# Optimization experiments

Hardware: AMD Instinct MI355X
Metric: run time of the kernel (lower is better)

## Reference

```python
import jax, jax.numpy as jnp
import numpy as np

B, HW, ENC, E, D, A, V, L = 64, 14, 2048, 512, 512, 512, 32000, 32
LN_EPS = 1e-5


def setup_inputs() -> dict:
    key = jax.random.key(0)
    ks = jax.random.split(key, 16)
    s = 0.02
    n = lambda k, sh: jax.random.normal(k, sh, jnp.float32)
    encoder_out = n(ks[0], (B, HW, HW, ENC))
    encoded_captions = jax.random.randint(ks[1], (B, L), 0, V)
    caption_lengths = jax.random.randint(ks[2], (B, 1), 2, L + 1)
    caption_lengths = caption_lengths.at[0, 0].set(L)  # ensure max length present
    return dict(
        encoder_out=encoder_out,
        encoded_captions=encoded_captions,
        caption_lengths=caption_lengths,
        emb=n(ks[3], (V, E)) * s,
        W_enc_att=n(ks[4], (A, ENC)) * s, b_enc_att=jnp.zeros((A,)),
        W_dec_att=n(ks[5], (A, D)) * s, b_dec_att=jnp.zeros((A,)),
        W_full_att=n(ks[6], (1, A)) * s, b_full_att=jnp.zeros((1,)),
        W_ih=n(ks[7], (4 * D, E + ENC)) * s, b_ih=jnp.zeros((4 * D,)),
        W_hh=n(ks[8], (4 * D, D)) * s, b_hh=jnp.zeros((4 * D,)),
        g_h=jnp.ones((D,)), be_h=jnp.zeros((D,)),
        g_c=jnp.ones((D,)), be_c=jnp.zeros((D,)),
        W_init_h=n(ks[9], (D, ENC)) * s, b_init_h=jnp.zeros((D,)),
        W_init_c=n(ks[10], (D, ENC)) * s, b_init_c=jnp.zeros((D,)),
        W_beta=n(ks[11], (ENC, D)) * s, b_beta=jnp.zeros((ENC,)),
        W_fc=n(ks[12], (V, D)) * s, b_fc=jnp.zeros((V,)),
    )


def _layer_norm(x, g, b):
    m = x.mean(-1, keepdims=True)
    v = ((x - m) ** 2).mean(-1, keepdims=True)
    return (x - m) / jnp.sqrt(v + LN_EPS) * g + b


def reference(encoder_out, encoded_captions, caption_lengths, emb,
              W_enc_att, b_enc_att, W_dec_att, b_dec_att, W_full_att, b_full_att,
              W_ih, b_ih, W_hh, b_hh, g_h, be_h, g_c, be_c,
              W_init_h, b_init_h, W_init_c, b_init_c, W_beta, b_beta, W_fc, b_fc):
    bsz = encoder_out.shape[0]
    enc_out = encoder_out.reshape(bsz, -1, encoder_out.shape[-1])  # [B,P,ENC]
    lengths = caption_lengths[:, 0]
    order = jnp.argsort(-lengths)  # stable descending sort (matches torch sort)
    lengths = lengths[order]
    enc_out = enc_out[order]
    caps = encoded_captions[order]
    embeds = emb[caps]  # [B,L,E]
    decode_lengths = lengths - 1
    T = caps.shape[1] - 1  # static max(decode_lengths)

    mean_enc = enc_out.mean(axis=1)
    h = _layer_norm(mean_enc @ W_init_h.T + b_init_h, g_h, be_h)
    c = _layer_norm(mean_enc @ W_init_c.T + b_init_c, g_c, be_c)

    att1 = enc_out @ W_enc_att.T + b_enc_att  # [B,P,A] precomputed once
    prev_seq = jnp.swapaxes(embeds[:, :T], 0, 1)  # [T,B,E] teacher-forced inputs
    masks = jnp.arange(T)[:, None] < decode_lengths[None, :]  # [T,B] active rows

    def step(carry, xs):
        h, c = carry
        prev, mask = xs
        # attention
        att2 = h @ W_dec_att.T + b_dec_att  # [B,A]
        e = jax.nn.relu(att1 + att2[:, None, :]) @ W_full_att[0] + b_full_att[0]  # [B,P]
        alpha = jax.nn.softmax(e, axis=1)
        awe = jnp.einsum('bpe,bp->be', enc_out, alpha)  # [B,ENC]
        gate = jax.nn.sigmoid(h @ W_beta.T + b_beta)
        awe = gate * awe
        # LSTM cell
        x = jnp.concatenate([prev, awe], axis=1)  # [B,E+ENC]
        gates = x @ W_ih.T + b_ih + h @ W_hh.T + b_hh
        i, f, g, o = jnp.split(gates, 4, axis=1)
        c_new = jax.nn.sigmoid(f) * c + jax.nn.sigmoid(i) * jnp.tanh(g)
        h_new = jax.nn.sigmoid(o) * jnp.tanh(c_new)
        h_new = _layer_norm(h_new, g_h, be_h)
        c_new = _layer_norm(c_new, g_c, be_c)
        preds = h_new @ W_fc.T + b_fc  # [B,V]; dropout is identity in eval
        m = mask[:, None]
        h = jnp.where(m, h_new, h)  # freeze finished rows (== torch batch shrink)
        c = jnp.where(m, c_new, c)
        return (h, c), (jnp.where(m, preds, 0.0), jnp.where(m, alpha, 0.0))

    (_, _), (preds_t, alphas_t) = jax.lax.scan(step, (h, c), (prev_seq, masks))
    predictions = jnp.swapaxes(preds_t, 0, 1)  # [B,T,V]
    alphas = jnp.swapaxes(alphas_t, 0, 1)      # [B,T,P]
    return predictions, caps, decode_lengths, alphas, order
```

## Files before the change

kernel.cpp:

```cpp
#include <hip/hip_runtime.h>
#include <cfloat>
#include <math.h>

#define B_ 64
#define P_ 196
#define ENC_ 2048
#define D_ 512
#define V_ 32000
#define L_ 32
#define T_ 31

#define OUT_PREDS 0L
#define OUT_CAPS  63488000L
#define OUT_DECL  63490048L
#define OUT_ALPH  63490112L
#define OUT_ORDER 63878976L

typedef __bf16 bf16;
typedef __bf16 bf16x8 __attribute__((ext_vector_type(8)));
typedef __bf16 bf16x4 __attribute__((ext_vector_type(4)));
typedef __bf16 bf16x2 __attribute__((ext_vector_type(2)));
typedef float  f32x4  __attribute__((ext_vector_type(4)));

static __device__ __forceinline__ float sigmoidf_(float x) { return 1.f / (1.f + __expf(-x)); }

__global__ void k_order(const int* __restrict__ cap_len, const int* __restrict__ caps,
                        int* __restrict__ order_i, int* __restrict__ declen_i,
                        int* __restrict__ caps_i, float* __restrict__ out,
                        int* __restrict__ rmap, int* __restrict__ orow, int* __restrict__ mact)
{
    __shared__ int len_s[B_], dl_s[B_];
    int tid = threadIdx.x;
    len_s[tid] = cap_len[tid];
    __syncthreads();
    int li = len_s[tid];
    int pos = 0;
    for (int j = 0; j < B_; ++j) {
        int lj = len_s[j];
        pos += (lj > li) || (lj == li && j < tid);
    }
    order_i[pos]  = tid;
    declen_i[pos] = li - 1;
    dl_s[pos]     = li - 1;
    out[OUT_ORDER + pos] = (float)tid;
    out[OUT_DECL  + pos] = (float)(li - 1);
    for (int l = 0; l < L_; ++l) {
        int tok = caps[tid * L_ + l];
        caps_i[pos * L_ + l] = tok;
        out[OUT_CAPS + pos * L_ + l] = (float)tok;
    }
    __syncthreads();
    int p = tid;
    int off = 0;
    for (int j = 0; j < p; ++j) off += dl_s[j];
    int dl = dl_s[p];
    for (int tt = 0; tt < dl; ++tt) {
        rmap[off + tt] = tt * B_ + p;
        orow[off + tt] = p * T_ + tt;
    }
    if (p == B_ - 1) {
        int M = off + dl;
        mact[0] = M;
        int Mr = (M + 63) & ~63;
        for (int i = M; i < Mr; ++i) { rmap[i] = 0; orow[i] = -1; }
    }
}

struct CvtSegs { const float* s[8]; bf16* d[8]; long cum[9]; };
__global__ __launch_bounds__(256) void k_cvt_all(CvtSegs cs)
{
    long i8 = ((long)blockIdx.x * 256 + threadIdx.x) * 8;
    if (i8 >= cs.cum[8]) return;
    int k = 0;
    while (i8 >= cs.cum[k + 1]) ++k;
    long loc = i8 - cs.cum[k];
    const float* src = cs.s[k] + loc;
    float4 a = *(const float4*)(src);
    float4 b = *(const float4*)(src + 4);
    bf16x8 v;
    v[0]=(bf16)a.x; v[1]=(bf16)a.y; v[2]=(bf16)a.z; v[3]=(bf16)a.w;
    v[4]=(bf16)b.x; v[5]=(bf16)b.y; v[6]=(bf16)b.z; v[7]=(bf16)b.w;
    *(bf16x8*)(cs.d[k] + loc) = v;
}

__global__ __launch_bounds__(256) void k_cvt_enc(const float* __restrict__ enc,
                                                 const int* __restrict__ order_i,
                                                 bf16* __restrict__ enc_s)
{
    long i = ((long)blockIdx.x * 256 + threadIdx.x) * 8;
    int b = (int)(i / ((long)P_ * ENC_));
    long rem = i - (long)b * P_ * ENC_;
    const float* src = enc + (long)order_i[b] * P_ * ENC_ + rem;
    float4 a = *(const float4*)(src);
    float4 c = *(const float4*)(src + 4);
    bf16x8 v;
    v[0]=(bf16)a.x; v[1]=(bf16)a.y; v[2]=(bf16)a.z; v[3]=(bf16)a.w;
    v[4]=(bf16)c.x; v[5]=(bf16)c.y; v[6]=(bf16)c.z; v[7]=(bf16)c.w;
    *(bf16x8*)(enc_s + i) = v;
}

__global__ __launch_bounds__(256) void k_meanb(const bf16* __restrict__ enc_s, bf16* __restrict__ mean_b)
{
    int b = blockIdx.x, col = blockIdx.y * 256 + threadIdx.x;
    float s = 0.f;
    const bf16* eb = enc_s + (long)b * P_ * ENC_ + col;
    for (int p = 0; p < P_; ++p) s += (float)eb[(long)p * ENC_];
    mean_b[(long)b * ENC_ + col] = (bf16)(s * (1.f / (float)P_));
}

template<int MI, int FUSE, int EPI, int SWZ>
__global__ void __launch_bounds__(256)
k_mgemm(const bf16* __restrict__ A, long lda,
        const bf16* __restrict__ B1, const bf16* __restrict__ B2,
        const float* __restrict__ bias,
        float* __restrict__ Cf, bf16* __restrict__ Cb,
        int N, int K, int kspl, int Nsp, int Ksp, int Mtot)
{
    const int tid = threadIdx.x;
    const int lane = tid & 63, w = tid >> 6;
    int mt, nt, z;
    if (SWZ == 0) { mt = blockIdx.x; nt = blockIdx.y; z = blockIdx.z; }
    else          { int o = blockIdx.x; int wg = (o & 7) * 196 + (o >> 3);
                    mt = wg >> 3; nt = (wg >> 1) & 3; z = wg & 1; }
    const int krange = K / kspl;
    const int k0 = z * krange, k1 = k0 + krange;
    const int r16 = lane & 15, kq = lane >> 4;
    const int koff = kq * 8;

    const bf16* Ap = A + (long)(mt * (MI * 16) + r16) * lda + koff;
    const int ncol0 = nt * 128 + w * 32;

    const bf16* Bp[2];
    const bf16* B2p[2];
#pragma unroll
    for (int ni = 0; ni < 2; ++ni) {
        int n = ncol0 + ni * 16 + r16;
        if (FUSE == 1)
            Bp[ni] = (n < Nsp) ? B1 + (long)n * K + koff
                               : B2 + (long)(n - Nsp) * K + koff;
        else if (FUSE == 2) {
            Bp[ni]  = B1 + (long)n * Ksp + koff;
            B2p[ni] = B2 + (long)n * (K - Ksp) + koff - Ksp;
        } else
            Bp[ni] = B1 + (long)n * K + koff;
    }

    auto loadA = [&](int kk, bf16x8* dst) {
#pragma unroll
        for (int mi = 0; mi < MI; ++mi)
            dst[mi] = *(const bf16x8*)(Ap + (long)mi * 16 * lda + kk);
    };
    auto loadB = [&](int kk, bf16x8* dst) {
#pragma unroll
        for (int ni = 0; ni < 2; ++ni) {
            if (FUSE == 2 && kk >= Ksp) dst[ni] = *(const bf16x8*)(B2p[ni] + kk);
            else                        dst[ni] = *(const bf16x8*)(Bp[ni] + kk);
        }
    };

    f32x4 acc[MI][2] = {};
    bf16x8 af[MI], bfr[2];
    loadA(k0, af); loadB(k0, bfr);
    for (int kk = k0 + 32; kk < k1; kk += 32) {
        bf16x8 af2[MI], bf2[2];
        loadA(kk, af2); loadB(kk, bf2);
#pragma unroll
        for (int mi = 0; mi < MI; ++mi)
#pragma unroll
            for (int ni = 0; ni < 2; ++ni)
                acc[mi][ni] = __builtin_amdgcn_mfma_f32_16x16x32_bf16(bfr[ni], af[mi], acc[mi][ni], 0, 0, 0);
#pragma unroll
        for (int mi = 0; mi < MI; ++mi) af[mi] = af2[mi];
#pragma unroll
        for (int ni = 0; ni < 2; ++ni) bfr[ni] = bf2[ni];
    }
#pragma unroll
    for (int mi = 0; mi < MI; ++mi)
#pragma unroll
        for (int ni = 0; ni < 2; ++ni)
            acc[mi][ni] = __builtin_amdgcn_mfma_f32_16x16x32_bf16(bfr[ni], af[mi], acc[mi][ni], 0, 0, 0);

#pragma unroll
    for (int mi = 0; mi < MI; ++mi) {
        const int row = mt * (MI * 16) + mi * 16 + r16;
#pragma unroll
        for (int ni = 0; ni < 2; ++ni) {
            const int col = ncol0 + ni * 16 + kq * 4;
            f32x4 v = acc[mi][ni];
            if (EPI == 0) {
                *(f32x4*)(Cf + (long)z * Mtot * N + (long)row * N + col) = v;
            } else {
                f32x4 bv = *(const f32x4*)(bias + col);
                bf16x4 o;
                o[0]=(bf16)(v[0]+bv[0]); o[1]=(bf16)(v[1]+bv[1]);
                o[2]=(bf16)(v[2]+bv[2]); o[3]=(bf16)(v[3]+bv[3]);
                *(bf16x4*)(Cb + (long)row * N + col) = o;
            }
        }
    }
}

__global__ __launch_bounds__(256)
void k_red(const float* __restrict__ p, const float* __restrict__ bias, bf16* __restrict__ ob)
{
    const long TOT = (long)12544 * 512;
    long i = ((long)blockIdx.x * 256 + threadIdx.x) * 8;
    f32x4 a0 = *(const f32x4*)(p + i);
    f32x4 a1 = *(const f32x4*)(p + i + 4);
    f32x4 b0 = *(const f32x4*)(p + TOT + i);
    f32x4 b1 = *(const f32x4*)(p + TOT + i + 4);
    int col = (int)(i & 511);
    f32x4 c0 = *(const f32x4*)(bias + col);
    f32x4 c1 = *(const f32x4*)(bias + col + 4);
    bf16x8 v;
    v[0]=(bf16)(a0[0]+b0[0]+c0[0]); v[1]=(bf16)(a0[1]+b0[1]+c0[1]);
    v[2]=(bf16)(a0[2]+b0[2]+c0[2]); v[3]=(bf16)(a0[3]+b0[3]+c0[3]);
    v[4]=(bf16)(a1[0]+b1[0]+c1[0]); v[5]=(bf16)(a1[1]+b1[1]+c1[1]);
    v[6]=(bf16)(a1[2]+b1[2]+c1[2]); v[7]=(bf16)(a1[3]+b1[3]+c1[3]);
    *(bf16x8*)(ob + i) = v;
}

__global__ __launch_bounds__(512)
void k_initln(const float* __restrict__ pi,
              const float* __restrict__ b_h, const float* __restrict__ b_c,
              const float* __restrict__ g_h, const float* __restrict__ be_h,
              const float* __restrict__ g_c, const float* __restrict__ be_c,
              bf16* __restrict__ xh, float* __restrict__ cbuf)
{
    int b = blockIdx.x, d = threadIdx.x;
    float yh = pi[(long)b * 1024 + d]       + b_h[d];
    float yc = pi[(long)b * 1024 + 512 + d] + b_c[d];
    __shared__ float r1[512], r2[512], r3[512], r4[512];
    r1[d] = yh; r2[d] = yh * yh; r3[d] = yc; r4[d] = yc * yc;
    __syncthreads();
    for (int s = 256; s > 0; s >>= 1) {
        if (d < s) { r1[d]+=r1[d+s]; r2[d]+=r2[d+s]; r3[d]+=r3[d+s]; r4[d]+=r4[d+s]; }
        __syncthreads();
    }
    float mh = r1[0] * (1.f/512.f), vh = r2[0] * (1.f/512.f) - mh*mh;
    float mc = r3[0] * (1.f/512.f), vc = r4[0] * (1.f/512.f) - mc*mc;
    float hln = (yh - mh) * rsqrtf(vh + 1e-5f) * g_h[d] + be_h[d];
    float cln = (yc - mc) * rsqrtf(vc + 1e-5f) * g_c[d] + be_c[d];
    xh[(long)b * 3072 + 2560 + d] = (bf16)hln;
    cbuf[(long)b * 512 + d] = cln;
}

__global__ __launch_bounds__(512)
void k_attn(const float* __restrict__ att2gate, const float* __restrict__ b_dec,
            const float* __restrict__ b_beta, const float* __restrict__ Wfull,
            const bf16* __restrict__ att1_b, const bf16* __restrict__ enc_s,
            const int* __restrict__ caps_i, const int* __restrict__ declen_i,
            const float* __restrict__ emb,
            bf16* __restrict__ xh, float* __restrict__ out, int t)
{
    const int b = blockIdx.x >> 1, seg = blockIdx.x & 1, tid = threadIdx.x;
    if (t >= declen_i[b]) {
        if (seg == 1 && tid < P_) out[OUT_ALPH + ((long)b * T_ + t) * P_ + tid] = 0.f;
        return;
    }
    __shared__ float att2s[512], wf[512], red[512], alp[P_];
    {
        float s = b_dec[tid];
#pragma unroll
        for (int zz = 0; zz < 4; ++zz) s += att2gate[((long)zz * 64 + b) * 2560 + tid];
        att2s[tid] = s;
        wf[tid] = Wfull[tid];
    }
    __syncthreads();
    float ev = -FLT_MAX;
    if (tid < P_) {
        const bf16* ar = att1_b + ((long)b * P_ + tid) * 512;
        float acc = 0.f;
        for (int a0 = 0; a0 < 512; a0 += 8) {
            bf16x8 v = *(const bf16x8*)(ar + a0);
#pragma unroll
            for (int j = 0; j < 8; ++j)
                acc += fmaxf((float)v[j] + att2s[a0 + j], 0.f) * wf[a0 + j];
        }
        ev = acc;
    }
    red[tid] = ev;
    __syncthreads();
    for (int s = 256; s > 0; s >>= 1) { if (tid < s) red[tid] = fmaxf(red[tid], red[tid + s]); __syncthreads(); }
    float mx = red[0];
    __syncthreads();
    float ex = (tid < P_) ? __expf(ev - mx) : 0.f;
    red[tid] = ex;
    __syncthreads();
    for (int s = 256; s > 0; s >>= 1) { if (tid < s) red[tid] += red[tid + s]; __syncthreads(); }
    float inv = 1.f / red[0];
    if (tid < P_) alp[tid] = ex * inv;
    __syncthreads();
    if (seg == 1 && tid < P_)
        out[OUT_ALPH + ((long)b * T_ + t) * P_ + tid] = alp[tid];
    const int c0 = seg * 1024 + tid * 2;
    const bf16* eb = enc_s + (long)b * P_ * ENC_ + c0;
    float a0 = 0.f, a1 = 0.f;
#pragma unroll 4
    for (int p = 0; p < P_; ++p) {
        bf16x2 v = *(const bf16x2*)(eb + (long)p * ENC_);
        float al = alp[p];
        a0 += al * (float)v[0]; a1 += al * (float)v[1];
    }
    float g0 = b_beta[c0], g1 = b_beta[c0 + 1];
#pragma unroll
    for (int zz = 0; zz < 4; ++zz) {
        const float* gs = att2gate + ((long)zz * 64 + b) * 2560 + 512 + c0;
        g0 += gs[0]; g1 += gs[1];
    }
    bf16x2 o;
    o[0] = (bf16)(a0 * sigmoidf_(g0));
    o[1] = (bf16)(a1 * sigmoidf_(g1));
    *(bf16x2*)(xh + (long)b * 3072 + 512 + c0) = o;
    if (seg == 0) {
        int tok = caps_i[b * L_ + t];
        xh[(long)b * 3072 + tid] = (bf16)emb[(long)tok * 512 + tid];
    }
}

__global__ __launch_bounds__(512)
void k_lstm(const float* __restrict__ gp, const float* __restrict__ b_ih, const float* __restrict__ b_hh,
            const float* __restrict__ g_h, const float* __restrict__ be_h,
            const float* __restrict__ g_c, const float* __restrict__ be_c,
            bf16* __restrict__ xh, float* __restrict__ cbuf, bf16* __restrict__ hseq,
            const int* __restrict__ declen_i, int t)
{
    int b = blockIdx.x, d = threadIdx.x;
    if (t >= declen_i[b]) return;
    float iv = b_ih[d]        + b_hh[d];
    float fv = b_ih[512 + d]  + b_hh[512 + d];
    float gv = b_ih[1024 + d] + b_hh[1024 + d];
    float ov = b_ih[1536 + d] + b_hh[1536 + d];
#pragma unroll
    for (int s = 0; s < 8; ++s) {
        const float* gs = gp + ((long)s * B_ + b) * 2048;
        iv += gs[d]; fv += gs[512 + d]; gv += gs[1024 + d]; ov += gs[1536 + d];
    }
    float cn = sigmoidf_(fv) * cbuf[(long)b * 512 + d] + sigmoidf_(iv) * tanhf(gv);
    float hn = sigmoidf_(ov) * tanhf(cn);
    __shared__ float r1[512], r2[512], r3[512], r4[512];
    r1[d] = hn; r2[d] = hn * hn; r3[d] = cn; r4[d] = cn * cn;
    __syncthreads();
    for (int s = 256; s > 0; s >>= 1) {
        if (d < s) { r1[d]+=r1[d+s]; r2[d]+=r2[d+s]; r3[d]+=r3[d+s]; r4[d]+=r4[d+s]; }
        __syncthreads();
    }
    float mh = r1[0] * (1.f/512.f), vh = r2[0] * (1.f/512.f) - mh*mh;
    float mc = r3[0] * (1.f/512.f), vc = r4[0] * (1.f/512.f) - mc*mc;
    float hln = (hn - mh) * rsqrtf(vh + 1e-5f) * g_h[d] + be_h[d];
    float cln = (cn - mc) * rsqrtf(vc + 1e-5f) * g_c[d] + be_c[d];
    bf16 hv = (bf16)hln;
    xh[(long)b * 3072 + 2560 + d] = hv;
    hseq[((long)t * B_ + b) * 512 + d] = hv;
    cbuf[(long)b * 512 + d] = cln;
}

__global__ __launch_bounds__(256) void k_zero(const int* __restrict__ declen_i, float* __restrict__ out)
{
    int x = blockIdx.x;
    int b = x / T_, t = x - b * T_;
    if (t < declen_i[b]) return;
    float4 z = {0.f, 0.f, 0.f, 0.f};
    long base = OUT_PREDS + ((long)b * T_ + t) * V_;
    for (int i = threadIdx.x * 4; i < V_; i += 1024)
        *(float4*)(out + base + i) = z;
}

__global__ __launch_bounds__(256)
void k_preds(const bf16* __restrict__ hseq, const bf16* __restrict__ Wfc,
             const float* __restrict__ bias,
             const int* __restrict__ rmap, const int* __restrict__ orow,
             const int* __restrict__ mact, float* __restrict__ out)
{
    int o = blockIdx.x; int xcd = o & 7;
    int base = xcd < 6 ? xcd * 969 : 5814 + (xcd - 6) * 968;
    int wg = base + (o >> 3);
    int nt = wg / 31, mt = wg - 31 * nt;
    if (mt * 64 >= mact[0]) return;
    __shared__ int rs[64], os[64];
    __shared__ __align__(16) float ct[64][132];
    const int tid = threadIdx.x, lane = tid & 63, w = tid >> 6;
    const int r16 = lane & 15, kq = lane >> 4, koff = kq * 8;
    if (tid < 64) { rs[tid] = rmap[mt * 64 + tid]; os[tid] = orow[mt * 64 + tid]; }
    __syncthreads();
    const int ncol0 = nt * 128 + w * 32;
    const bf16* Ap[4];
#pragma unroll
    for (int mi = 0; mi < 4; ++mi)
        Ap[mi] = hseq + (long)rs[mi * 16 + r16] * 512 + koff;
    const bf16* Bp[2];
#pragma unroll
    for (int ni = 0; ni < 2; ++ni)
        Bp[ni] = Wfc + (long)(ncol0 + ni * 16 + r16) * 512 + koff;

    f32x4 acc[4][2] = {};
    bf16x8 af[4], bfr[2];
#pragma unroll
    for (int mi = 0; mi < 4; ++mi) af[mi] = *(const bf16x8*)(Ap[mi]);
#pragma unroll
    for (int ni = 0; ni < 2; ++ni) bfr[ni] = *(const bf16x8*)(Bp[ni]);
    for (int kk = 32; kk < 512; kk += 32) {
        bf16x8 af2[4], bf2[2];
#pragma unroll
        for (int mi = 0; mi < 4; ++mi) af2[mi] = *(const bf16x8*)(Ap[mi] + kk);
#pragma unroll
        for (int ni = 0; ni < 2; ++ni) bf2[ni] = *(const bf16x8*)(Bp[ni] + kk);
#pragma unroll
        for (int mi = 0; mi < 4; ++mi)
#pragma unroll
            for (int ni = 0; ni < 2; ++ni)
                acc[mi][ni] = __builtin_amdgcn_mfma_f32_16x16x32_bf16(bfr[ni], af[mi], acc[mi][ni], 0, 0, 0);
#pragma unroll
        for (int mi = 0; mi < 4; ++mi) af[mi] = af2[mi];
#pragma unroll
        for (int ni = 0; ni < 2; ++ni) bfr[ni] = bf2[ni];
    }
#pragma unroll
    for (int mi = 0; mi < 4; ++mi)
#pragma unroll
        for (int ni = 0; ni < 2; ++ni)
            acc[mi][ni] = __builtin_amdgcn_mfma_f32_16x16x32_bf16(bfr[ni], af[mi], acc[mi][ni], 0, 0, 0);

#pragma unroll
    for (int mi = 0; mi < 4; ++mi)
#pragma unroll
        for (int ni = 0; ni < 2; ++ni)
            *(f32x4*)&ct[mi * 16 + r16][w * 32 + ni * 16 + kq * 4] = acc[mi][ni];
    __syncthreads();
    const int r0 = tid >> 5, cc = (tid & 31) * 4;
    const int gcol = nt * 128 + cc;
    f32x4 bv = *(const f32x4*)(bias + gcol);
#pragma unroll
    for (int it = 0; it < 8; ++it) {
        int r = it * 8 + r0;
        int orv = os[r];
        if (orv >= 0) {
            f32x4 v = *(f32x4*)&ct[r][cc];
            f32x4 oo;
            oo[0] = v[0] + bv[0]; oo[1] = v[1] + bv[1];
            oo[2] = v[2] + bv[2]; oo[3] = v[3] + bv[3];
            *(f32x4*)(out + OUT_PREDS + (long)orv * V_ + gcol) = oo;
        }
    }
}

extern "C" void kernel_launch(void* const* d_in, const int* in_sizes, int n_in,
                              void* d_out, int out_size, void* d_ws, size_t ws_size,
                              hipStream_t stream)
{
    const float* enc       = (const float*)d_in[0];
    const int*   caps      = (const int*)  d_in[1];
    const int*   caplen    = (const int*)  d_in[2];
    const float* emb       = (const float*)d_in[3];
    const float* W_enc_att = (const float*)d_in[4];
    const float* b_enc_att = (const float*)d_in[5];
    const float* W_dec_att = (const float*)d_in[6];
    const float* b_dec_att = (const float*)d_in[7];
    const float* W_full    = (const float*)d_in[8];
    const float* W_ih      = (const float*)d_in[10];
    const float* b_ih      = (const float*)d_in[11];
    const float* W_hh      = (const float*)d_in[12];
    const float* b_hh      = (const float*)d_in[13];
    const float* g_h       = (const float*)d_in[14];
    const float* be_h      = (const float*)d_in[15];
    const float* g_c       = (const float*)d_in[16];
    const float* be_c      = (const float*)d_in[17];
    const float* W_init_h  = (const float*)d_in[18];
    const float* b_init_h  = (const float*)d_in[19];
    const float* W_init_c  = (const float*)d_in[20];
    const float* b_init_c  = (const float*)d_in[21];
    const float* W_beta    = (const float*)d_in[22];
    const float* b_beta    = (const float*)d_in[23];
    const float* W_fc      = (const float*)d_in[24];
    const float* b_fc      = (const float*)d_in[25];
    float* out = (float*)d_out;

    char* w = (char*)d_ws;
    auto alloc = [&](size_t bytes) { char* p = w; w += (bytes + 255) & ~(size_t)255; return p; };
    int*   order_i  = (int*)  alloc(B_ * 4);
    int*   declen_i = (int*)  alloc(B_ * 4);
    int*   caps_i   = (int*)  alloc(B_ * L_ * 4);
    int*   rmap     = (int*)  alloc(2048 * 4);
    int*   orow     = (int*)  alloc(2048 * 4);
    int*   mact     = (int*)  alloc(256);
    bf16*  enc_s    = (bf16*) alloc((size_t)B_ * P_ * ENC_ * 2);
    bf16*  mean_b   = (bf16*) alloc((size_t)B_ * ENC_ * 2);
    bf16*  att1_b   = (bf16*) alloc((size_t)B_ * P_ * 512 * 2);
    float* pi       = (float*)alloc((size_t)B_ * 1024 * 4);
    float* cbuf     = (float*)alloc((size_t)B_ * 512 * 4);
    bf16*  xh       = (bf16*) alloc((size_t)B_ * 3072 * 2);
    float* att1_p   = (float*)alloc((size_t)2 * 12544 * 512 * 4);
    float* gp       = att1_p;
    float* att2gate = (float*)((char*)att1_p + ((size_t)8 * B_ * 2048 * 4 + 255 & ~(size_t)255));
    bf16*  hseq     = (bf16*)((char*)att2gate + ((size_t)4 * B_ * 2560 * 4 + 255 & ~(size_t)255));
    bf16*  W_enc_b  = (bf16*) alloc((size_t)512 * 2048 * 2);
    bf16*  W_dec_b  = (bf16*) alloc((size_t)512 * 512 * 2);
    bf16*  W_beta_b = (bf16*) alloc((size_t)2048 * 512 * 2);
    bf16*  W_ih_b   = (bf16*) alloc((size_t)2048 * 2560 * 2);
    bf16*  W_hh_b   = (bf16*) alloc((size_t)2048 * 512 * 2);
    bf16*  W_fc_b   = (bf16*) alloc((size_t)32000 * 512 * 2);
    bf16*  W_inh_b  = (bf16*) alloc((size_t)512 * 2048 * 2);
    bf16*  W_inc_b  = (bf16*) alloc((size_t)512 * 2048 * 2);

    k_order<<<1, B_, 0, stream>>>(caplen, caps, order_i, declen_i, caps_i, out, rmap, orow, mact);
    k_cvt_enc<<<12544, 256, 0, stream>>>(enc, order_i, enc_s);
    k_meanb<<<dim3(B_, 8), 256, 0, stream>>>(enc_s, mean_b);

    CvtSegs cs;
    const float* srcs[8] = {W_enc_att, W_dec_att, W_beta, W_ih, W_hh, W_fc, W_init_h, W_init_c};
    bf16* dsts[8] = {W_enc_b, W_dec_b, W_beta_b, W_ih_b, W_hh_b, W_fc_b, W_inh_b, W_inc_b};
    long ns[8] = {512L*2048, 512L*512, 2048L*512, 2048L*2560, 2048L*512, 32000L*512, 512L*2048, 512L*2048};
    long cum = 0;
    for (int i = 0; i < 8; ++i) { cs.s[i] = srcs[i]; cs.d[i] = dsts[i]; cs.cum[i] = cum; cum += ns[i]; }
    cs.cum[8] = cum;
    k_cvt_all<<<(int)((cum / 8 + 255) / 256), 256, 0, stream>>>(cs);

    k_mgemm<4, 1, 0, 0><<<dim3(1, 8, 1), 256, 0, stream>>>(mean_b, 2048, W_inh_b, W_inc_b,
        nullptr, pi, nullptr, 1024, 2048, 1, 512, 0, 64);
    k_initln<<<B_, 512, 0, stream>>>(pi, b_init_h, b_init_c, g_h, be_h, g_c, be_c, xh, cbuf);

    k_mgemm<4, 0, 0, 1><<<1568, 256, 0, stream>>>(enc_s, 2048, W_enc_b, nullptr,
        nullptr, att1_p, nullptr, 512, 2048, 2, 0, 0, 12544);
    k_red<<<3136, 256, 0, stream>>>(att1_p, b_enc_att, att1_b);

    for (int t = 0; t < T_; ++t) {
        k_mgemm<4, 1, 0, 0><<<dim3(1, 20, 4), 256, 0, stream>>>(xh + 2560, 3072, W_dec_b, W_beta_b,
            nullptr, att2gate, nullptr, 2560, 512, 4, 512, 0, 64);
        k_attn<<<128, 512, 0, stream>>>(att2gate, b_dec_att, b_beta, W_full, att1_b, enc_s,
            caps_i, declen_i, emb, xh, out, t);
        k_mgemm<4, 2, 0, 0><<<dim3(1, 16, 8), 256, 0, stream>>>(xh, 3072, W_ih_b, W_hh_b,
            nullptr, gp, nullptr, 2048, 3072, 8, 0, 2560, 64);
        k_lstm<<<B_, 512, 0, stream>>>(gp, b_ih, b_hh, g_h, be_h, g_c, be_c,
            xh, cbuf, hseq, declen_i, t);
    }

    k_zero<<<B_ * T_, 256, 0, stream>>>(declen_i, out);
    k_preds<<<7750, 256, 0, stream>>>(hseq, W_fc_b, b_fc, rmap, orow, mact, out);
}
```

Measured before the change: 2.258 ms.

## Pre-pack weights into MFMA tile layout, fuse zero-fill into preds, drop split-K for att1

Weights for the attention/gate, LSTM and fc GEMMs are converted to bf16 directly into a tile-packed layout, so each lane's 8-element fragment loads are contiguous within a 16-row tile. The gathered decoder hidden states are also packed per 64-row tile before the vocabulary projection. The separate zero-fill kernel is folded into k_preds via encoded negative row indices, and the encoder attention GEMM now runs with MI=8 and no split-K, writing bf16 with bias directly instead of going through an fp32 partial buffer and a reduction kernel. This cuts memory traffic and launches, but adds packing kernels and leaves fewer, larger blocks for the att1 GEMM.

```diff
diff --git a/kernel.cpp b/kernel.cpp
--- a/kernel.cpp
+++ b/kernel.cpp
@@ -30,6 +30,7 @@
                         int* __restrict__ rmap, int* __restrict__ orow, int* __restrict__ mact)
 {
     __shared__ int len_s[B_], dl_s[B_];
+    __shared__ int Msh;
     int tid = threadIdx.x;
     len_s[tid] = cap_len[tid];
     __syncthreads();
@@ -54,23 +55,24 @@
     int off = 0;
     for (int j = 0; j < p; ++j) off += dl_s[j];
     int dl = dl_s[p];
+    if (p == B_ - 1) { Msh = off + dl; mact[0] = off + dl; }
+    __syncthreads();
     for (int tt = 0; tt < dl; ++tt) {
         rmap[off + tt] = tt * B_ + p;
         orow[off + tt] = p * T_ + tt;
     }
-    if (p == B_ - 1) {
-        int M = off + dl;
-        mact[0] = M;
-        int Mr = (M + 63) & ~63;
-        for (int i = M; i < Mr; ++i) { rmap[i] = 0; orow[i] = -1; }
-    }
-}
-
-struct CvtSegs { const float* s[8]; bf16* d[8]; long cum[9]; };
+    int ibase = Msh + p * T_ - off;
+    for (int tt = dl; tt < T_; ++tt) {
+        rmap[ibase + (tt - dl)] = 0;
+        orow[ibase + (tt - dl)] = -(p * T_ + tt) - 1;
+    }
+}
+
+struct CvtSegs { const float* s[3]; bf16* d[3]; long cum[4]; };
 __global__ __launch_bounds__(256) void k_cvt_all(CvtSegs cs)
 {
     long i8 = ((long)blockIdx.x * 256 + threadIdx.x) * 8;
-    if (i8 >= cs.cum[8]) return;
+    if (i8 >= cs.cum[3]) return;
     int k = 0;
     while (i8 >= cs.cum[k + 1]) ++k;
     long loc = i8 - cs.cum[k];
@@ -83,6 +85,45 @@
     *(bf16x8*)(cs.d[k] + loc) = v;
 }
 
+template<int MODE>
+__global__ __launch_bounds__(256)
+void k_packB(const float* __restrict__ s1, const float* __restrict__ s2,
+             bf16* __restrict__ dst, int Kv, int Nsp, int Ksp)
+{
+    const int ntile = blockIdx.x, tid = threadIdx.x;
+    long tbase = (long)ntile * Kv * 16;
+    const int groups = Kv * 2;
+    for (int g = tid; g < groups; g += 256) {
+        int kkq = g >> 4, r16 = g & 15;
+        int n = ntile * 16 + r16, k0 = kkq * 8;
+        const float* src;
+        if (MODE == 0)      src = s1 + (long)n * Kv + k0;
+        else if (MODE == 1) src = (n < Nsp) ? s1 + (long)n * Kv + k0
+                                            : s2 + (long)(n - Nsp) * Kv + k0;
+        else                src = (k0 < Ksp) ? s1 + (long)n * Ksp + k0
+                                             : s2 + (long)n * (Kv - Ksp) + (k0 - Ksp);
+        float4 a = *(const float4*)src;
+        float4 b = *(const float4*)(src + 4);
+        bf16x8 v;
+        v[0]=(bf16)a.x; v[1]=(bf16)a.y; v[2]=(bf16)a.z; v[3]=(bf16)a.w;
+        v[4]=(bf16)b.x; v[5]=(bf16)b.y; v[6]=(bf16)b.z; v[7]=(bf16)b.w;
+        *(bf16x8*)(dst + tbase + (long)kkq * 128 + r16 * 8) = v;
+    }
+}
+
+__global__ __launch_bounds__(256)
+void k_packA(const bf16* __restrict__ hseq, const int* __restrict__ rmap, bf16* __restrict__ dst)
+{
+    const int mt = blockIdx.x, tid = threadIdx.x;
+    long tbase = (long)mt * 32768;
+    for (int g = tid; g < 4096; g += 256) {
+        int mi = g >> 10, rem = g & 1023, kkq = rem >> 4, r16 = rem & 15;
+        int row = rmap[mt * 64 + mi * 16 + r16];
+        bf16x8 v = *(const bf16x8*)(hseq + (long)row * 512 + kkq * 8);
+        *(bf16x8*)(dst + tbase + mi * 8192 + (long)kkq * 128 + r16 * 8) = v;
+    }
+}
+
 __global__ __launch_bounds__(256) void k_cvt_enc(const float* __restrict__ enc,
                                                  const int* __restrict__ order_i,
                                                  bf16* __restrict__ enc_s)
@@ -108,20 +149,20 @@
     mean_b[(long)b * ENC_ + col] = (bf16)(s * (1.f / (float)P_));
 }
 
-template<int MI, int FUSE, int EPI, int SWZ>
+template<int MI, int FUSE, int EPI, int SWZ, int PK>
 __global__ void __launch_bounds__(256)
 k_mgemm(const bf16* __restrict__ A, long lda,
         const bf16* __restrict__ B1, const bf16* __restrict__ B2,
         const float* __restrict__ bias,
         float* __restrict__ Cf, bf16* __restrict__ Cb,
-        int N, int K, int kspl, int Nsp, int Ksp, int Mtot)
+        int N, int K, int kspl, int Nsp, int Mtot)
 {
     const int tid = threadIdx.x;
     const int lane = tid & 63, w = tid >> 6;
     int mt, nt, z;
     if (SWZ == 0) { mt = blockIdx.x; nt = blockIdx.y; z = blockIdx.z; }
-    else          { int o = blockIdx.x; int wg = (o & 7) * 196 + (o >> 3);
-                    mt = wg >> 3; nt = (wg >> 1) & 3; z = wg & 1; }
+    else          { int o = blockIdx.x; int wg = (o & 7) * 49 + (o >> 3);
+                    mt = wg >> 2; nt = wg & 3; z = 0; }
     const int krange = K / kspl;
     const int k0 = z * krange, k1 = k0 + krange;
     const int r16 = lane & 15, kq = lane >> 4;
@@ -131,18 +172,18 @@
     const int ncol0 = nt * 128 + w * 32;
 
     const bf16* Bp[2];
-    const bf16* B2p[2];
 #pragma unroll
     for (int ni = 0; ni < 2; ++ni) {
-        int n = ncol0 + ni * 16 + r16;
-        if (FUSE == 1)
-            Bp[ni] = (n < Nsp) ? B1 + (long)n * K + koff
-                               : B2 + (long)(n - Nsp) * K + koff;
-        else if (FUSE == 2) {
-            Bp[ni]  = B1 + (long)n * Ksp + koff;
-            B2p[ni] = B2 + (long)n * (K - Ksp) + koff - Ksp;
-        } else
-            Bp[ni] = B1 + (long)n * K + koff;
+        if (PK) {
+            Bp[ni] = B1 + (long)((ncol0 + ni * 16) >> 4) * ((long)K * 16) + kq * 128 + r16 * 8;
+        } else {
+            int n = ncol0 + ni * 16 + r16;
+            if (FUSE == 1)
+                Bp[ni] = (n < Nsp) ? B1 + (long)n * K + koff
+                                   : B2 + (long)(n - Nsp) * K + koff;
+            else
+                Bp[ni] = B1 + (long)n * K + koff;
+        }
     }
 
     auto loadA = [&](int kk, bf16x8* dst) {
@@ -152,10 +193,9 @@
     };
     auto loadB = [&](int kk, bf16x8* dst) {
 #pragma unroll
-        for (int ni = 0; ni < 2; ++ni) {
-            if (FUSE == 2 && kk >= Ksp) dst[ni] = *(const bf16x8*)(B2p[ni] + kk);
-            else                        dst[ni] = *(const bf16x8*)(Bp[ni] + kk);
-        }
+        for (int ni = 0; ni < 2; ++ni)
+            dst[ni] = PK ? *(const bf16x8*)(Bp[ni] + (long)kk * 16)
+                         : *(const bf16x8*)(Bp[ni] + kk);
     };
 
     f32x4 acc[MI][2] = {};
@@ -200,26 +240,6 @@
     }
 }
 
-__global__ __launch_bounds__(256)
-void k_red(const float* __restrict__ p, const float* __restrict__ bias, bf16* __restrict__ ob)
-{
-    const long TOT = (long)12544 * 512;
-    long i = ((long)blockIdx.x * 256 + threadIdx.x) * 8;
-    f32x4 a0 = *(const f32x4*)(p + i);
-    f32x4 a1 = *(const f32x4*)(p + i + 4);
-    f32x4 b0 = *(const f32x4*)(p + TOT + i);
-    f32x4 b1 = *(const f32x4*)(p + TOT + i + 4);
-    int col = (int)(i & 511);
-    f32x4 c0 = *(const f32x4*)(bias + col);
-    f32x4 c1 = *(const f32x4*)(bias + col + 4);
-    bf16x8 v;
-    v[0]=(bf16)(a0[0]+b0[0]+c0[0]); v[1]=(bf16)(a0[1]+b0[1]+c0[1]);
-    v[2]=(bf16)(a0[2]+b0[2]+c0[2]); v[3]=(bf16)(a0[3]+b0[3]+c0[3]);
-    v[4]=(bf16)(a1[0]+b1[0]+c1[0]); v[5]=(bf16)(a1[1]+b1[1]+c1[1]);
-    v[6]=(bf16)(a1[2]+b1[2]+c1[2]); v[7]=(bf16)(a1[3]+b1[3]+c1[3]);
-    *(bf16x8*)(ob + i) = v;
-}
-
 __global__ __launch_bounds__(512)
 void k_initln(const float* __restrict__ pi,
               const float* __restrict__ b_h, const float* __restrict__ b_c,
@@ -355,43 +375,41 @@
     cbuf[(long)b * 512 + d] = cln;
 }
 
-__global__ __launch_bounds__(256) void k_zero(const int* __restrict__ declen_i, float* __restrict__ out)
-{
-    int x = blockIdx.x;
-    int b = x / T_, t = x - b * T_;
-    if (t < declen_i[b]) return;
-    float4 z = {0.f, 0.f, 0.f, 0.f};
-    long base = OUT_PREDS + ((long)b * T_ + t) * V_;
-    for (int i = threadIdx.x * 4; i < V_; i += 1024)
-        *(float4*)(out + base + i) = z;
-}
-
 __global__ __launch_bounds__(256)
-void k_preds(const bf16* __restrict__ hseq, const bf16* __restrict__ Wfc,
-             const float* __restrict__ bias,
-             const int* __restrict__ rmap, const int* __restrict__ orow,
+void k_preds(const bf16* __restrict__ Apk, const bf16* __restrict__ Bpk,
+             const float* __restrict__ bias, const int* __restrict__ orow,
              const int* __restrict__ mact, float* __restrict__ out)
 {
     int o = blockIdx.x; int xcd = o & 7;
     int base = xcd < 6 ? xcd * 969 : 5814 + (xcd - 6) * 968;
     int wg = base + (o >> 3);
     int nt = wg / 31, mt = wg - 31 * nt;
-    if (mt * 64 >= mact[0]) return;
-    __shared__ int rs[64], os[64];
+    __shared__ int os[64];
     __shared__ __align__(16) float ct[64][132];
     const int tid = threadIdx.x, lane = tid & 63, w = tid >> 6;
-    const int r16 = lane & 15, kq = lane >> 4, koff = kq * 8;
-    if (tid < 64) { rs[tid] = rmap[mt * 64 + tid]; os[tid] = orow[mt * 64 + tid]; }
-    __syncthreads();
-    const int ncol0 = nt * 128 + w * 32;
+    const int r16 = lane & 15, kq = lane >> 4;
+    if (tid < 64) os[tid] = orow[mt * 64 + tid];
+    __syncthreads();
+    const int r0 = tid >> 5, cc = (tid & 31) * 4;
+    const int gcol = nt * 128 + cc;
+    if (mt * 64 >= mact[0]) {
+        f32x4 zz = {0.f, 0.f, 0.f, 0.f};
+#pragma unroll
+        for (int it = 0; it < 8; ++it) {
+            int r = it * 8 + r0;
+            int row = -os[r] - 1;
+            *(f32x4*)(out + OUT_PREDS + (long)row * V_ + gcol) = zz;
+        }
+        return;
+    }
     const bf16* Ap[4];
 #pragma unroll
     for (int mi = 0; mi < 4; ++mi)
-        Ap[mi] = hseq + (long)rs[mi * 16 + r16] * 512 + koff;
+        Ap[mi] = Apk + (long)mt * 32768 + mi * 8192 + kq * 128 + r16 * 8;
     const bf16* Bp[2];
 #pragma unroll
     for (int ni = 0; ni < 2; ++ni)
-        Bp[ni] = Wfc + (long)(ncol0 + ni * 16 + r16) * 512 + koff;
+        Bp[ni] = Bpk + (long)((nt * 128 + w * 32 + ni * 16) >> 4) * 8192 + kq * 128 + r16 * 8;
 
     f32x4 acc[4][2] = {};
     bf16x8 af[4], bfr[2];
@@ -402,9 +420,9 @@
     for (int kk = 32; kk < 512; kk += 32) {
         bf16x8 af2[4], bf2[2];
 #pragma unroll
-        for (int mi = 0; mi < 4; ++mi) af2[mi] = *(const bf16x8*)(Ap[mi] + kk);
-#pragma unroll
-        for (int ni = 0; ni < 2; ++ni) bf2[ni] = *(const bf16x8*)(Bp[ni] + kk);
+        for (int mi = 0; mi < 4; ++mi) af2[mi] = *(const bf16x8*)(Ap[mi] + kk * 16);
+#pragma unroll
+        for (int ni = 0; ni < 2; ++ni) bf2[ni] = *(const bf16x8*)(Bp[ni] + kk * 16);
 #pragma unroll
         for (int mi = 0; mi < 4; ++mi)
 #pragma unroll
@@ -427,9 +445,8 @@
         for (int ni = 0; ni < 2; ++ni)
             *(f32x4*)&ct[mi * 16 + r16][w * 32 + ni * 16 + kq * 4] = acc[mi][ni];
     __syncthreads();
-    const int r0 = tid >> 5, cc = (tid & 31) * 4;
-    const int gcol = nt * 128 + cc;
     f32x4 bv = *(const f32x4*)(bias + gcol);
+    f32x4 zz = {0.f, 0.f, 0.f, 0.f};
 #pragma unroll
     for (int it = 0; it < 8; ++it) {
         int r = it * 8 + r0;
@@ -440,6 +457,9 @@
             oo[0] = v[0] + bv[0]; oo[1] = v[1] + bv[1];
             oo[2] = v[2] + bv[2]; oo[3] = v[3] + bv[3];
             *(f32x4*)(out + OUT_PREDS + (long)orv * V_ + gcol) = oo;
+        } else {
+            int row = -orv - 1;
+            *(f32x4*)(out + OUT_PREDS + (long)row * V_ + gcol) = zz;
         }
     }
 }
@@ -489,51 +509,52 @@
     float* pi       = (float*)alloc((size_t)B_ * 1024 * 4);
     float* cbuf     = (float*)alloc((size_t)B_ * 512 * 4);
     bf16*  xh       = (bf16*) alloc((size_t)B_ * 3072 * 2);
-    float* att1_p   = (float*)alloc((size_t)2 * 12544 * 512 * 4);
-    float* gp       = att1_p;
-    float* att2gate = (float*)((char*)att1_p + ((size_t)8 * B_ * 2048 * 4 + 255 & ~(size_t)255));
-    bf16*  hseq     = (bf16*)((char*)att2gate + ((size_t)4 * B_ * 2560 * 4 + 255 & ~(size_t)255));
+    float* att2gate = (float*)alloc((size_t)4 * B_ * 2560 * 4);
+    float* gp       = (float*)alloc((size_t)8 * B_ * 2048 * 4);
+    bf16*  hseq     = (bf16*) alloc((size_t)T_ * B_ * 512 * 2);
+    bf16*  Apk      = (bf16*) alloc((size_t)31 * 32768 * 2);
     bf16*  W_enc_b  = (bf16*) alloc((size_t)512 * 2048 * 2);
-    bf16*  W_dec_b  = (bf16*) alloc((size_t)512 * 512 * 2);
-    bf16*  W_beta_b = (bf16*) alloc((size_t)2048 * 512 * 2);
-    bf16*  W_ih_b   = (bf16*) alloc((size_t)2048 * 2560 * 2);
-    bf16*  W_hh_b   = (bf16*) alloc((size_t)2048 * 512 * 2);
-    bf16*  W_fc_b   = (bf16*) alloc((size_t)32000 * 512 * 2);
     bf16*  W_inh_b  = (bf16*) alloc((size_t)512 * 2048 * 2);
     bf16*  W_inc_b  = (bf16*) alloc((size_t)512 * 2048 * 2);
+    bf16*  Wab_pk   = (bf16*) alloc((size_t)2560 * 512 * 2);
+    bf16*  Wg_pk    = (bf16*) alloc((size_t)2048 * 3072 * 2);
+    bf16*  Wfc_pk   = (bf16*) alloc((size_t)32000 * 512 * 2);
 
     k_order<<<1, B_, 0, stream>>>(caplen, caps, order_i, declen_i, caps_i, out, rmap, orow, mact);
     k_cvt_enc<<<12544, 256, 0, stream>>>(enc, order_i, enc_s);
     k_meanb<<<dim3(B_, 8), 256, 0, stream>>>(enc_s, mean_b);
 
     CvtSegs cs;
-    const float* srcs[8] = {W_enc_att, W_dec_att, W_beta, W_ih, W_hh, W_fc, W_init_h, W_init_c};
-    bf16* dsts[8] = {W_enc_b, W_dec_b, W_beta_b, W_ih_b, W_hh_b, W_fc_b, W_inh_b, W_inc_b};
-    long ns[8] = {512L*2048, 512L*512, 2048L*512, 2048L*2560, 2048L*512, 32000L*512, 512L*2048, 512L*2048};
+    const float* srcs[3] = {W_enc_att, W_init_h, W_init_c};
+    bf16* dsts[3] = {W_enc_b, W_inh_b, W_inc_b};
+    long ns[3] = {512L*2048, 512L*2048, 512L*2048};
     long cum = 0;
-    for (int i = 0; i < 8; ++i) { cs.s[i] = srcs[i]; cs.d[i] = dsts[i]; cs.cum[i] = cum; cum += ns[i]; }
-    cs.cum[8] = cum;
+    for (int i = 0; i < 3; ++i) { cs.s[i] = srcs[i]; cs.d[i] = dsts[i]; cs.cum[i] = cum; cum += ns[i]; }
+    cs.cum[3] = cum;
     k_cvt_all<<<(int)((cum / 8 + 255) / 256), 256, 0, stream>>>(cs);
 
-    k_mgemm<4, 1, 0, 0><<<dim3(1, 8, 1), 256, 0, stream>>>(mean_b, 2048, W_inh_b, W_inc_b,
-        nullptr, pi, nullptr, 1024, 2048, 1, 512, 0, 64);
+    k_packB<1><<<160, 256, 0, stream>>>(W_dec_att, W_beta, Wab_pk, 512, 512, 0);
+    k_packB<2><<<128, 256, 0, stream>>>(W_ih, W_hh, Wg_pk, 3072, 0, 2560);
+    k_packB<0><<<2000, 256, 0, stream>>>(W_fc, nullptr, Wfc_pk, 512, 0, 0);
+
+    k_mgemm<4, 1, 0, 0, 0><<<dim3(1, 8, 1), 256, 0, stream>>>(mean_b, 2048, W_inh_b, W_inc_b,
+        nullptr, pi, nullptr, 1024, 2048, 1, 512, 64);
     k_initln<<<B_, 512, 0, stream>>>(pi, b_init_h, b_init_c, g_h, be_h, g_c, be_c, xh, cbuf);
 
-    k_mgemm<4, 0, 0, 1><<<1568, 256, 0, stream>>>(enc_s, 2048, W_enc_b, nullptr,
-        nullptr, att1_p, nullptr, 512, 2048, 2, 0, 0, 12544);
-    k_red<<<3136, 256, 0, stream>>>(att1_p, b_enc_att, att1_b);
+    k_mgemm<8, 0, 1, 1, 0><<<392, 256, 0, stream>>>(enc_s, 2048, W_enc_b, nullptr,
+        b_enc_att, nullptr, att1_b, 512, 2048, 1, 0, 12544);
 
     for (int t = 0; t < T_; ++t) {
-        k_mgemm<4, 1, 0, 0><<<dim3(1, 20, 4), 256, 0, stream>>>(xh + 2560, 3072, W_dec_b, W_beta_b,
-            nullptr, att2gate, nullptr, 2560, 512, 4, 512, 0, 64);
+        k_mgemm<4, 0, 0, 0, 1><<<dim3(1, 20, 4), 256, 0, stream>>>(xh + 2560, 3072, Wab_pk, nullptr,
+            nullptr, att2gate, nullptr, 2560, 512, 4, 0, 64);
         k_attn<<<128, 512, 0, stream>>>(att2gate, b_dec_att, b_beta, W_full, att1_b, enc_s,
             caps_i, declen_i, emb, xh, out, t);
-        k_mgemm<4, 2, 0, 0><<<dim3(1, 16, 8), 256, 0, stream>>>(xh, 3072, W_ih_b, W_hh_b,
-            nullptr, gp, nullptr, 2048, 3072, 8, 0, 2560, 64);
+        k_mgemm<4, 0, 0, 0, 1><<<dim3(1, 16, 8), 256, 0, stream>>>(xh, 3072, Wg_pk, nullptr,
+            nullptr, gp, nullptr, 2048, 3072, 8, 0, 64);
         k_lstm<<<B_, 512, 0, stream>>>(gp, b_ih, b_hh, g_h, be_h, g_c, be_c,
             xh, cbuf, hseq, declen_i, t);
     }
 
-    k_zero<<<B_ * T_, 256, 0, stream>>>(declen_i, out);
-    k_preds<<<7750, 256, 0, stream>>>(hseq, W_fc_b, b_fc, rmap, orow, mact, out);
-}
+    k_packA<<<31, 256, 0, stream>>>(hseq, rmap, Apk);
+    k_preds<<<7750, 256, 0, stream>>>(Apk, Wfc_pk, b_fc, orow, mact, out);
+}
```

Result: faster. 2.086 ms (-7.6%).
